# Kernel tuning notes

Measured on AMD Instinct MI355X. Metric: run time of the kernel, lower is better.

## Reference

```python
import jax, jax.numpy as jnp
import numpy as np

# ---- static config (mirrors init_kwargs) ----
B, A, NC = 16, 3, 80          # batch, anchors-per-head, classes
W = H = 76                     # grid (inputwidth / stride-8)
INPUTW = 608.0
M = 32                         # GT boxes per image
IGNORE = 0.5                   # ignore_thresh
MASK_N = 3                     # mask = [0,1,2] -> first 3 anchors belong to this head
ANCHORS = np.array([[10,13],[16,30],[33,23],[30,61],[62,45],[59,119],
                    [116,90],[156,198],[373,326]], dtype=np.float32)


def _box_iou(b1, b2):
    """b1 [N,4], b2 [P,4] xyxy -> iou [N,P] (same math as torch box_iou)."""
    area1 = (b1[:, 2] - b1[:, 0]) * (b1[:, 3] - b1[:, 1])
    area2 = (b2[:, 2] - b2[:, 0]) * (b2[:, 3] - b2[:, 1])
    lt = jnp.maximum(b1[:, None, :2], b2[None, :, :2])
    rb = jnp.minimum(b1[:, None, 2:], b2[None, :, 2:])
    inter = jnp.clip(rb - lt, 0.0).prod(-1)
    return inter / (area1[:, None] + area2[None, :] - inter)


def setup_inputs() -> dict:
    key = jax.random.key(0)
    k1, k2, k3, k4 = jax.random.split(key, 4)
    prediction = jax.random.normal(k1, (B, A * (5 + NC), W, H), jnp.float32) * 0.5
    # gt rows: (label, cx, cy, w, h, batch_idx), normalized coords, sorted by image
    labels = jax.random.randint(k2, (B * M, 1), 0, NC).astype(jnp.float32)
    cxy = jax.random.uniform(k3, (B * M, 2), minval=0.15, maxval=0.85)
    wh = jax.random.uniform(k4, (B * M, 2), minval=0.05, maxval=0.30)
    bidx = jnp.repeat(jnp.arange(B, dtype=jnp.float32), M)[:, None]
    gt = jnp.concatenate([labels, cxy, wh, bidx], axis=1)
    return {"prediction": prediction, "gt": gt}


def reference(prediction, gt):
    p = prediction.reshape(B, A, W, H, 5 + NC)
    cxp = jax.nn.sigmoid(p[..., 0])
    cyp = jax.nn.sigmoid(p[..., 1])
    wp, hp = p[..., 2], p[..., 3]
    confp = jax.nn.sigmoid(p[..., 4])
    classesp = jax.nn.sigmoid(p[..., 5:])
    # decode (anchors_g are the ORIGINAL pixel anchors: assigned before /strides)
    aw = jnp.asarray(ANCHORS[:MASK_N, 0]).reshape(1, A, 1, 1)
    ah = jnp.asarray(ANCHORS[:MASK_N, 1]).reshape(1, A, 1, 1)
    predx = cxp + jnp.arange(W, dtype=p.dtype)[None, None, None, :]
    predy = cyp + jnp.arange(H, dtype=p.dtype)[None, None, :, None]
    predw = jnp.exp(wp) * aw / INPUTW * W
    predh = jnp.exp(hp) * ah / INPUTW * H
    decoded = jnp.concatenate([predx[..., None], predy[..., None], predw[..., None],
                               predh[..., None], confp[..., None], classesp], axis=-1)

    # predicted boxes in pixel xyxy, flattened per image: [B, A*W*H, 4]
    x1 = (predx - predw * 0.5) / W * INPUTW
    y1 = (predy - predh * 0.5) / H * INPUTW
    x2 = (predx + predw * 0.5) / W * INPUTW
    y2 = (predy + predh * 0.5) / H * INPUTW
    pr = jnp.stack([x1, y1, x2, y2], axis=-1).reshape(B, -1, 4)

    # GT boxes per image (fixed M per image, rows sorted by batch idx)
    gtb = gt.reshape(B, M, 6)
    cx, cy, gw, gh = gtb[..., 1], gtb[..., 2], gtb[..., 3], gtb[..., 4]
    gxyxy = jnp.stack([(cx - gw * 0.5) * INPUTW, (cy - gh * 0.5) * INPUTW,
                       (cx + gw * 0.5) * INPUTW, (cy + gh * 0.5) * INPUTW], axis=-1)

    # per-image GT x all-preds IoU; noobj where best IoU <= ignore_thresh
    iou = jax.vmap(_box_iou)(gxyxy, pr)            # [B, M, A*W*H]
    maxv = iou.max(axis=1).reshape(B, A, H, W)      # W==H so flat order matches
    noobj = maxv <= IGNORE

    # best-anchor assignment per GT (vs all 9 anchors centered at the GT)
    ori = jnp.asarray(ANCHORS) / INPUTW             # [9,2] normalized
    fcx, fcy = cx.reshape(-1), cy.reshape(-1)       # [B*M]
    gflat = gxyxy.reshape(-1, 4)
    abox = jnp.stack([(fcx[:, None] - ori[None, :, 0] * 0.5) * INPUTW,
                      (fcy[:, None] - ori[None, :, 1] * 0.5) * INPUTW,
                      (fcx[:, None] + ori[None, :, 0] * 0.5) * INPUTW,
                      (fcy[:, None] + ori[None, :, 1] * 0.5) * INPUTW], axis=-1)  # [BM,9,4]
    lt = jnp.maximum(gflat[:, None, :2], abox[..., :2])
    rb = jnp.minimum(gflat[:, None, 2:], abox[..., 2:])
    inter = jnp.clip(rb - lt, 0.0).prod(-1)
    area_g = (gflat[:, 2] - gflat[:, 0]) * (gflat[:, 3] - gflat[:, 1])
    area_a = (abox[..., 2] - abox[..., 0]) * (abox[..., 3] - abox[..., 1])
    g_a = inter / (area_g[:, None] + area_a - inter)   # [BM,9]
    best = jnp.argmax(g_a, axis=1)
    valid = best < MASK_N                               # mask=[0,1,2] -> a_ind == best
    a_ind = jnp.clip(best, 0, MASK_N - 1)
    gi = (fcx * W).astype(jnp.int32)                    # original indexes dim-2 with x*width
    gj = (fcy * H).astype(jnp.int32)
    bb = jnp.repeat(jnp.arange(B), M)
    flat = ((bb * A + a_ind) * H + gi) * W + gj
    obj = jnp.zeros(B * A * H * W, bool).at[flat].max(valid).reshape(B, A, H, W)
    noobj = noobj.reshape(-1).at[flat].min(~valid).reshape(B, A, H, W)
    return decoded, noobj, obj
```

## Files before the change

kernel.cpp:

```cpp
#include <hip/hip_runtime.h>
#include <math.h>

#define BB 16
#define AA 3
#define NCC 80
#define WW 76
#define MM 32
#define CELLS_PER_IMG (AA * WW * WW)
#define NDECODE (BB * CELLS_PER_IMG * 85)
#define NCELLS (BB * CELLS_PER_IMG)

typedef float vfloat4 __attribute__((ext_vector_type(4)));

__constant__ float c_anchor[9][2] = {
    {10.f,13.f},{16.f,30.f},{33.f,23.f},{30.f,61.f},{62.f,45.f},
    {59.f,119.f},{116.f,90.f},{156.f,198.f},{373.f,326.f}};

#define LOG2E 1.4426950408889634f

__device__ __forceinline__ float fast_sigmoid(float x) {
    return __builtin_amdgcn_rcpf(1.0f + __builtin_amdgcn_exp2f(-x * LOG2E));
}

__global__ void bulk_sigmoid_kernel(const vfloat4* __restrict__ in, vfloat4* __restrict__ out) {
    const int n4 = NDECODE / 4;
    int tid = blockIdx.x * blockDim.x + threadIdx.x;
    if (tid >= n4) return;
    vfloat4 v = in[tid];
    vfloat4 o;
    o.x = fast_sigmoid(v.x);
    o.y = fast_sigmoid(v.y);
    o.z = fast_sigmoid(v.z);
    o.w = fast_sigmoid(v.w);
    out[tid] = o;
}

__global__ void noobj_fixup_kernel(const float* __restrict__ in, const float* __restrict__ gt,
                                   float* __restrict__ out,
                                   float* __restrict__ noobj, float* __restrict__ obj) {
    __shared__ float4 sbox[MM];
    int b = blockIdx.y;
    int t = threadIdx.x;
    if (t < MM) {
        const float* g = gt + (size_t)(b * MM + t) * 6;
        float cx = g[1], cy = g[2], gw = g[3], gh = g[4];
        sbox[t] = make_float4((cx - gw * 0.5f) * 608.0f, (cy - gh * 0.5f) * 608.0f,
                              (cx + gw * 0.5f) * 608.0f, (cy + gh * 0.5f) * 608.0f);
    }
    __syncthreads();
    int n = blockIdx.x * blockDim.x + t;
    if (n >= CELLS_PER_IMG) return;
    size_t cell = (size_t)b * CELLS_PER_IMG + n;

    const float* ip = in + cell * 85;
    int h = n % WW;
    int w = (n / WW) % WW;
    int a = n / (WW * WW);
    float px = fast_sigmoid(ip[0]) + (float)h;
    float py = fast_sigmoid(ip[1]) + (float)w;
    float pw = __builtin_amdgcn_exp2f(ip[2] * LOG2E) * (c_anchor[a][0] * 0.125f);
    float ph = __builtin_amdgcn_exp2f(ip[3] * LOG2E) * (c_anchor[a][1] * 0.125f);
    float* op = out + cell * 85;
    op[0] = px; op[1] = py; op[2] = pw; op[3] = ph;

    float x1 = (px - pw * 0.5f) / 76.0f * 608.0f;
    float y1 = (py - ph * 0.5f) / 76.0f * 608.0f;
    float x2 = (px + pw * 0.5f) / 76.0f * 608.0f;
    float y2 = (py + ph * 0.5f) / 76.0f * 608.0f;
    float area2 = (x2 - x1) * (y2 - y1);
    float best = 0.0f;
#pragma unroll
    for (int m = 0; m < MM; ++m) {
        float4 gb = sbox[m];
        float area1 = (gb.z - gb.x) * (gb.w - gb.y);
        float ltx = fmaxf(gb.x, x1), lty = fmaxf(gb.y, y1);
        float rbx = fminf(gb.z, x2), rby = fminf(gb.w, y2);
        float inter = fmaxf(rbx - ltx, 0.0f) * fmaxf(rby - lty, 0.0f);
        float iou = inter * __builtin_amdgcn_rcpf(area1 + area2 - inter);
        best = fmaxf(best, iou);
    }
    noobj[cell] = (best <= 0.5f) ? 1.0f : 0.0f;
    obj[cell] = 0.0f;
}

__global__ void assign_kernel(const float* __restrict__ gt,
                              float* __restrict__ noobj, float* __restrict__ obj) {
    int r = blockIdx.x * blockDim.x + threadIdx.x;
    if (r >= BB * MM) return;
    const float* g = gt + (size_t)r * 6;
    float cx = g[1], cy = g[2], gw = g[3], gh = g[4];
    float gx1 = (cx - gw * 0.5f) * 608.0f, gy1 = (cy - gh * 0.5f) * 608.0f;
    float gx2 = (cx + gw * 0.5f) * 608.0f, gy2 = (cy + gh * 0.5f) * 608.0f;
    float area_g = (gx2 - gx1) * (gy2 - gy1);
    int best = 0;
    float bestv = -1.0f;
#pragma unroll
    for (int k = 0; k < 9; ++k) {
        float ow = c_anchor[k][0] / 608.0f, oh = c_anchor[k][1] / 608.0f;
        float ax1 = (cx - ow * 0.5f) * 608.0f, ay1 = (cy - oh * 0.5f) * 608.0f;
        float ax2 = (cx + ow * 0.5f) * 608.0f, ay2 = (cy + oh * 0.5f) * 608.0f;
        float ltx = fmaxf(gx1, ax1), lty = fmaxf(gy1, ay1);
        float rbx = fminf(gx2, ax2), rby = fminf(gy2, ay2);
        float inter = fmaxf(rbx - ltx, 0.0f) * fmaxf(rby - lty, 0.0f);
        float area_a = (ax2 - ax1) * (ay2 - ay1);
        float v = inter / (area_g + area_a - inter);
        if (v > bestv) { bestv = v; best = k; }
    }
    if (best < AA) {
        int b = r / MM;
        int gi = (int)(cx * 76.0f);
        int gj = (int)(cy * 76.0f);
        int flat = ((b * AA + best) * WW + gi) * WW + gj;
        obj[flat] = 1.0f;
        noobj[flat] = 0.0f;
    }
}

extern "C" void kernel_launch(void* const* d_in, const int* in_sizes, int n_in,
                              void* d_out, int out_size, void* d_ws, size_t ws_size,
                              hipStream_t stream) {
    const float* pred = (const float*)d_in[0];
    const float* gt   = (const float*)d_in[1];
    float* dec   = (float*)d_out;
    float* noobj = dec + NDECODE;
    float* obj   = noobj + NCELLS;

    const int n4 = NDECODE / 4;
    bulk_sigmoid_kernel<<<(n4 + 255) / 256, 256, 0, stream>>>(
        (const vfloat4*)pred, (vfloat4*)dec);

    dim3 gb((CELLS_PER_IMG + 255) / 256, BB);
    noobj_fixup_kernel<<<gb, 256, 0, stream>>>(pred, gt, dec, noobj, obj);

    assign_kernel<<<2, 256, 0, stream>>>(gt, noobj, obj);
}
```

Measured before the change: 206.7 us.

## Fuse bulk sigmoid pass and per-cell decode/IoU into one kernel

```diff
diff --git a/kernel.cpp b/kernel.cpp
--- a/kernel.cpp
+++ b/kernel.cpp
@@ -9,6 +9,9 @@
 #define CELLS_PER_IMG (AA * WW * WW)
 #define NDECODE (BB * CELLS_PER_IMG * 85)
 #define NCELLS (BB * CELLS_PER_IMG)
+
+#define CPB 24
+#define V4PB 510
 
 typedef float vfloat4 __attribute__((ext_vector_type(4)));
 
@@ -22,37 +25,48 @@
     return __builtin_amdgcn_rcpf(1.0f + __builtin_amdgcn_exp2f(-x * LOG2E));
 }
 
-__global__ void bulk_sigmoid_kernel(const vfloat4* __restrict__ in, vfloat4* __restrict__ out) {
-    const int n4 = NDECODE / 4;
-    int tid = blockIdx.x * blockDim.x + threadIdx.x;
-    if (tid >= n4) return;
-    vfloat4 v = in[tid];
-    vfloat4 o;
-    o.x = fast_sigmoid(v.x);
-    o.y = fast_sigmoid(v.y);
-    o.z = fast_sigmoid(v.z);
-    o.w = fast_sigmoid(v.w);
-    out[tid] = o;
-}
+__global__ void fused_decode_noobj_kernel(const float* __restrict__ pred,
+                                          const float* __restrict__ gt,
+                                          float* __restrict__ dec,
+                                          float* __restrict__ noobj,
+                                          float* __restrict__ obj) {
+    __shared__ float4 sbox[MM];
+    const int blk = blockIdx.x;
+    const int t = threadIdx.x;
+    const int b = blk / 722;
+    const int n0 = (blk - b * 722) * CPB;
+    const size_t cell0 = (size_t)b * CELLS_PER_IMG + n0;
 
-__global__ void noobj_fixup_kernel(const float* __restrict__ in, const float* __restrict__ gt,
-                                   float* __restrict__ out,
-                                   float* __restrict__ noobj, float* __restrict__ obj) {
-    __shared__ float4 sbox[MM];
-    int b = blockIdx.y;
-    int t = threadIdx.x;
     if (t < MM) {
         const float* g = gt + (size_t)(b * MM + t) * 6;
         float cx = g[1], cy = g[2], gw = g[3], gh = g[4];
         sbox[t] = make_float4((cx - gw * 0.5f) * 608.0f, (cy - gh * 0.5f) * 608.0f,
                               (cx + gw * 0.5f) * 608.0f, (cy + gh * 0.5f) * 608.0f);
     }
+
+    const vfloat4* in4 = (const vfloat4*)pred + cell0 * 85 / 4;
+    vfloat4* out4 = (vfloat4*)dec + cell0 * 85 / 4;
+    {
+        vfloat4 v = in4[t];
+        vfloat4 o;
+        o.x = fast_sigmoid(v.x); o.y = fast_sigmoid(v.y);
+        o.z = fast_sigmoid(v.z); o.w = fast_sigmoid(v.w);
+        out4[t] = o;
+        int i1 = t + 256;
+        if (i1 < V4PB) {
+            vfloat4 v2 = in4[i1];
+            vfloat4 o2;
+            o2.x = fast_sigmoid(v2.x); o2.y = fast_sigmoid(v2.y);
+            o2.z = fast_sigmoid(v2.z); o2.w = fast_sigmoid(v2.w);
+            out4[i1] = o2;
+        }
+    }
     __syncthreads();
-    int n = blockIdx.x * blockDim.x + t;
-    if (n >= CELLS_PER_IMG) return;
-    size_t cell = (size_t)b * CELLS_PER_IMG + n;
 
-    const float* ip = in + cell * 85;
+    if (t >= CPB) return;
+    int n = n0 + t;
+    size_t cell = cell0 + t;
+    const float* ip = pred + cell * 85;
     int h = n % WW;
     int w = (n / WW) % WW;
     int a = n / (WW * WW);
@@ -60,7 +74,7 @@
     float py = fast_sigmoid(ip[1]) + (float)w;
     float pw = __builtin_amdgcn_exp2f(ip[2] * LOG2E) * (c_anchor[a][0] * 0.125f);
     float ph = __builtin_amdgcn_exp2f(ip[3] * LOG2E) * (c_anchor[a][1] * 0.125f);
-    float* op = out + cell * 85;
+    float* op = dec + cell * 85;
     op[0] = px; op[1] = py; op[2] = pw; op[3] = ph;
 
     float x1 = (px - pw * 0.5f) / 76.0f * 608.0f;
@@ -125,12 +139,6 @@
     float* noobj = dec + NDECODE;
     float* obj   = noobj + NCELLS;
 
-    const int n4 = NDECODE / 4;
-    bulk_sigmoid_kernel<<<(n4 + 255) / 256, 256, 0, stream>>>(
-        (const vfloat4*)pred, (vfloat4*)dec);
-
-    dim3 gb((CELLS_PER_IMG + 255) / 256, BB);
-    noobj_fixup_kernel<<<gb, 256, 0, stream>>>(pred, gt, dec, noobj, obj);
-
+    fused_decode_noobj_kernel<<<NCELLS / CPB, 256, 0, stream>>>(pred, gt, dec, noobj, obj);
     assign_kernel<<<2, 256, 0, stream>>>(gt, noobj, obj);
 }
```

Result: slower. 211.7 us (+2.4%).
